# Optimization experiments

Hardware: AMD Instinct MI355X
Metric: run time of the kernel (lower is better)

## Reference

```python
import jax, jax.numpy as jnp
import numpy as np

N = 50000      # nodes
F_IN = 256     # nfeat
HID = 64       # nhid (per-head, layer 1)
H = 4          # heads layer 1
OUT = 64       # nhid2 (layer 2, heads=1, concat=False)
E = 800000     # edges (self-loops appended in reference)
NEG_SLOPE = 0.2  # PyG GATConv default LeakyReLU slope


def setup_inputs() -> dict:
    key = jax.random.key(0)
    ks = jax.random.split(key, 10)
    x = jax.random.normal(ks[0], (N, F_IN), dtype=jnp.float32)
    adj = jax.random.randint(ks[1], (2, E), 0, N)
    s1 = 1.0 / np.sqrt(F_IN)
    s2 = 1.0 / np.sqrt(H * HID)
    W1 = (jax.random.normal(ks[2], (F_IN, H * HID), dtype=jnp.float32) * s1)
    att_src1 = jax.random.normal(ks[3], (H, HID), dtype=jnp.float32) * 0.1
    att_dst1 = jax.random.normal(ks[4], (H, HID), dtype=jnp.float32) * 0.1
    b1 = jnp.zeros((H * HID,), dtype=jnp.float32)
    W2 = (jax.random.normal(ks[5], (H * HID, OUT), dtype=jnp.float32) * s2)
    att_src2 = jax.random.normal(ks[6], (1, OUT), dtype=jnp.float32) * 0.1
    att_dst2 = jax.random.normal(ks[7], (1, OUT), dtype=jnp.float32) * 0.1
    b2 = jnp.zeros((OUT,), dtype=jnp.float32)
    return {"x": x, "adj": adj, "W1": W1, "att_src1": att_src1,
            "att_dst1": att_dst1, "b1": b1, "W2": W2, "att_src2": att_src2,
            "att_dst2": att_dst2, "b2": b2}


def _gat_conv(x, src, dst, W, a_src, a_dst, bias, heads, out_ch, concat):
    n = x.shape[0]
    h = (x @ W).reshape(n, heads, out_ch)                    # [N, H, C]
    alpha_src = jnp.einsum('nhc,hc->nh', h, a_src)           # [N, H]
    alpha_dst = jnp.einsum('nhc,hc->nh', h, a_dst)           # [N, H]
    alpha = jax.nn.leaky_relu(alpha_src[src] + alpha_dst[dst],
                              negative_slope=NEG_SLOPE)      # [E, H]
    # segment softmax over incoming edges of each dst node
    m = jax.ops.segment_max(alpha, dst, num_segments=n)      # [N, H]
    e = jnp.exp(alpha - m[dst])
    denom = jax.ops.segment_sum(e, dst, num_segments=n)      # [N, H]
    a = e / denom[dst]                                       # [E, H]
    msg = h[src] * a[:, :, None]                             # [E, H, C]
    out = jax.ops.segment_sum(msg, dst, num_segments=n)      # [N, H, C]
    if concat:
        out = out.reshape(n, heads * out_ch)
    else:
        out = out.mean(axis=1)
    return out + bias


def reference(x, adj, W1, att_src1, att_dst1, b1, W2, att_src2, att_dst2, b2):
    loops = jnp.arange(N, dtype=adj.dtype)
    src = jnp.concatenate([adj[0], loops])
    dst = jnp.concatenate([adj[1], loops])
    h = _gat_conv(x, src, dst, W1, att_src1, att_dst1, b1, H, HID, True)
    h = jax.nn.elu(h)
    out = _gat_conv(h, src, dst, W2, att_src2, att_dst2, b2, 1, OUT, False)
    return jax.nn.log_softmax(out, axis=1)
```

## Files before the change

### kernel.cpp

```cpp
#include <hip/hip_runtime.h>
#include <cstdint>
#include <cstddef>

#define NN    50000
#define EE    800000
#define SLOPE 0.2f
#define MT64  782
#define CAP   64

#define NBIN  196
#define DSH   8
#define PBLK  1024
#define EPB   782
#define BCAP  14
#define OCAP  8192

typedef unsigned short ushortT;
typedef __attribute__((ext_vector_type(8))) short short8;
typedef __attribute__((ext_vector_type(4))) float floatx4;

__device__ __forceinline__ float lrelu(float x){ return x > 0.f ? x : SLOPE * x; }
__device__ __forceinline__ float eluf(float x){ return x > 0.f ? x : __expf(x) - 1.f; }
__device__ __forceinline__ ushortT f2b(float f){ unsigned u = __float_as_uint(f); u += 0x7fff + ((u >> 16) & 1); return (ushortT)(u >> 16); }
__device__ __forceinline__ float   b2f(ushortT b){ return __uint_as_float(((unsigned)b) << 16); }

__global__ __launch_bounds__(256) void castW_k(const float* __restrict__ W1, const float* __restrict__ W2,
                                               ushortT* __restrict__ W1T, ushortT* __restrict__ W2T,
                                               int* __restrict__ ovfcnt)
{
    int k = blockIdx.x, t = threadIdx.x;
    W1T[t * 256 + k] = f2b(W1[k * 256 + t]);
    if (t < 64) W2T[t * 256 + k] = f2b(W2[k * 64 + t]);
    if (k == 0 && t == 0) *ovfcnt = 0;
}

__global__ __launch_bounds__(256, 3) void gemmbin_k(const float* __restrict__ x,
                                                    const ushortT* __restrict__ W1T,
                                                    const float* __restrict__ attS,
                                                    const float* __restrict__ attD,
                                                    ushortT* __restrict__ h1b,
                                                    float* __restrict__ asrc,
                                                    float* __restrict__ adst,
                                                    const int* __restrict__ srcA,
                                                    const int* __restrict__ dstA,
                                                    unsigned* __restrict__ binned,
                                                    ushortT* __restrict__ cnt2,
                                                    unsigned* __restrict__ ovf,
                                                    int* __restrict__ ovfcnt)
{
    __shared__ int      hist[NBIN];
    __shared__ unsigned lrec[NBIN][BCAP];

    if (blockIdx.x >= MT64) {
        const int blk = blockIdx.x - MT64;
        const int tid = threadIdx.x;
        for (int i = tid; i < NBIN; i += 256) hist[i] = 0;
        __syncthreads();

        const int e0 = blk * EPB;
        const int e1 = min(e0 + EPB, EE);
        for (int e = e0 + tid; e < e1; e += 256) {
            int s = srcA[e], d = dstA[e];
            int bin = d >> DSH;
            unsigned rec = ((unsigned)s << DSH) | (unsigned)(d & 255);
            int r = atomicAdd(&hist[bin], 1);
            if (r < BCAP) lrec[bin][r] = rec;
            else {
                int o = atomicAdd(ovfcnt, 1);
                if (o < OCAP) ovf[o] = ((unsigned)s << 16) | (unsigned)d;
            }
        }
        __syncthreads();

        for (int b = tid; b < NBIN; b += 256)
            cnt2[(size_t)blk * NBIN + b] = (ushortT)min(hist[b], BCAP);
        for (int sIdx = tid; sIdx < NBIN * BCAP; sIdx += 256) {
            int b = sIdx / BCAP;
            int i = sIdx - b * BCAP;
            if (i < min(hist[b], BCAP))
                binned[((size_t)blk * NBIN + b) * BCAP + i] = lrec[b][i];
        }
        return;
    }

    const int tid  = threadIdx.x;
    const int w    = tid >> 6;
    const int lane = tid & 63;
    const int m16  = lane & 15;
    const int quad = lane >> 4;
    const int wr   = w >> 1;
    const int wc   = w & 1;
    const int rowbase = blockIdx.x * 64 + wr * 32;
    const int colbase = wc * 128;

    const long r0 = min(rowbase + m16,      NN - 1);
    const long r1 = min(rowbase + 16 + m16, NN - 1);
    const float* a0p = x + r0 * 256 + quad * 8;
    const float* a1p = x + r1 * 256 + quad * 8;
    const ushortT* bp0 = W1T + (size_t)(colbase + m16) * 256 + quad * 8;

    floatx4 acc[2][8];
    #pragma unroll
    for (int i = 0; i < 2; ++i)
        #pragma unroll
        for (int j = 0; j < 8; ++j) acc[i][j] = (floatx4){0.f, 0.f, 0.f, 0.f};

    #pragma unroll
    for (int it = 0; it < 8; ++it) {
        const int k0 = it * 32;
        float4 fa00 = *(const float4*)(a0p + k0);
        float4 fa01 = *(const float4*)(a0p + k0 + 4);
        float4 fa10 = *(const float4*)(a1p + k0);
        float4 fa11 = *(const float4*)(a1p + k0 + 4);
        uint4 fb[8];
        #pragma unroll
        for (int j = 0; j < 8; ++j)
            fb[j] = *(const uint4*)(bp0 + (size_t)j * 16 * 256 + k0);

        ushortT a16[16];
        a16[0]=f2b(fa00.x); a16[1]=f2b(fa00.y); a16[2]=f2b(fa00.z); a16[3]=f2b(fa00.w);
        a16[4]=f2b(fa01.x); a16[5]=f2b(fa01.y); a16[6]=f2b(fa01.z); a16[7]=f2b(fa01.w);
        a16[8]=f2b(fa10.x); a16[9]=f2b(fa10.y); a16[10]=f2b(fa10.z); a16[11]=f2b(fa10.w);
        a16[12]=f2b(fa11.x); a16[13]=f2b(fa11.y); a16[14]=f2b(fa11.z); a16[15]=f2b(fa11.w);
        short8 af0 = *(short8*)(a16);
        short8 af1 = *(short8*)(a16 + 8);

        #pragma unroll
        for (int j = 0; j < 8; ++j) {
            short8 bf = *(short8*)(&fb[j]);
            acc[0][j] = __builtin_amdgcn_mfma_f32_16x16x32_bf16(af0, bf, acc[0][j], 0, 0, 0);
            acc[1][j] = __builtin_amdgcn_mfma_f32_16x16x32_bf16(af1, bf, acc[1][j], 0, 0, 0);
        }
    }

    float attSv[8], attDv[8];
    #pragma unroll
    for (int j = 0; j < 8; ++j) {
        attSv[j] = attS[colbase + j * 16 + m16];
        attDv[j] = attD[colbase + j * 16 + m16];
    }

    #pragma unroll
    for (int i = 0; i < 2; ++i) {
        #pragma unroll
        for (int r = 0; r < 4; ++r) {
            int row = rowbase + i * 16 + quad * 4 + r;
            bool ok = row < NN;
            if (ok) {
                #pragma unroll
                for (int j = 0; j < 8; ++j)
                    h1b[(size_t)row * 256 + colbase + j * 16 + m16] = f2b(acc[i][j][r]);
            }
            float d0 = 0.f, d1 = 0.f, e0 = 0.f, e1 = 0.f;
            #pragma unroll
            for (int jj = 0; jj < 4; ++jj) {
                d0 += acc[i][jj][r]     * attSv[jj];
                e0 += acc[i][jj][r]     * attDv[jj];
                d1 += acc[i][jj + 4][r] * attSv[jj + 4];
                e1 += acc[i][jj + 4][r] * attDv[jj + 4];
            }
            #pragma unroll
            for (int off = 1; off < 16; off <<= 1) {
                d0 += __shfl_xor(d0, off); e0 += __shfl_xor(e0, off);
                d1 += __shfl_xor(d1, off); e1 += __shfl_xor(e1, off);
            }
            if (ok && m16 == 0) {
                int hb = row * 4 + wc * 2;
                asrc[hb] = d0; asrc[hb + 1] = d1;
                adst[hb] = e0; adst[hb + 1] = e1;
            }
        }
    }
}

__global__ __launch_bounds__(256) void bucket_k(const unsigned* __restrict__ binned,
                                                const ushortT* __restrict__ cnt2,
                                                const unsigned* __restrict__ ovf,
                                                const int* __restrict__ ovfcnt,
                                                ushortT* __restrict__ esorted,
                                                int* __restrict__ cnt)
{
    __shared__ ushortT c2[PBLK];
    __shared__ int     lcnt[256];
    __shared__ ushortT lbuck[256][CAP];
    const int b = blockIdx.x;
    const int tid = threadIdx.x;

    lcnt[tid] = 0;
    for (int i = tid; i < PBLK; i += 256) c2[i] = cnt2[(size_t)i * NBIN + b];
    __syncthreads();

    for (int s0 = tid; s0 < PBLK * BCAP; s0 += 1024) {
        unsigned recs[4]; int ok[4];
        #pragma unroll
        for (int q = 0; q < 4; ++q) {
            int s = s0 + q * 256;
            int blk = s / BCAP;
            int i = s - blk * BCAP;
            ok[q] = (i < (int)c2[blk]);
            recs[q] = ok[q] ? binned[((size_t)blk * NBIN + b) * BCAP + i] : 0u;
        }
        #pragma unroll
        for (int q = 0; q < 4; ++q) {
            if (ok[q]) {
                int dl = recs[q] & 255;
                int r = atomicAdd(&lcnt[dl], 1);
                if (r < CAP) lbuck[dl][r] = (ushortT)(recs[q] >> DSH);
            }
        }
    }

    int nov = *ovfcnt;
    nov = nov > OCAP ? OCAP : nov;
    for (int i = tid; i < nov; i += 256) {
        unsigned rec = ovf[i];
        int d = rec & 0xFFFF;
        if ((d >> DSH) == b) {
            int r = atomicAdd(&lcnt[d & 255], 1);
            if (r < CAP) lbuck[d & 255][r] = (ushortT)(rec >> 16);
        }
    }
    __syncthreads();

    const int nbase = b << DSH;
    {
        int n = nbase + tid;
        if (n < NN) cnt[n] = lcnt[tid];
    }
    unsigned* ed = (unsigned*)(esorted + (size_t)nbase * CAP);
    const unsigned* ls = (const unsigned*)(&lbuck[0][0]);
    for (int i = tid; i < 256 * (CAP / 2); i += 256) {
        if (nbase + (i >> 5) < NN) ed[i] = ls[i];
    }
}

__global__ __launch_bounds__(256) void gemm2_k(const ushortT* __restrict__ a2b,
                                               const ushortT* __restrict__ W2T,
                                               const float* __restrict__ attS,
                                               const float* __restrict__ attD,
                                               ushortT* __restrict__ t2b,
                                               float* __restrict__ asrc,
                                               float* __restrict__ adst)
{
    const int tid  = threadIdx.x;
    const int w    = tid >> 6;
    const int lane = tid & 63;
    const int m16  = lane & 15;
    const int quad = lane >> 4;
    const int rowbase = blockIdx.x * 64 + w * 16;

    const long r0 = min(rowbase + m16, NN - 1);
    const ushortT* ap  = a2b + r0 * 256 + quad * 8;
    const ushortT* bp0 = W2T + (size_t)m16 * 256 + quad * 8;

    floatx4 acc[4];
    #pragma unroll
    for (int j = 0; j < 4; ++j) acc[j] = (floatx4){0.f, 0.f, 0.f, 0.f};

    #pragma unroll
    for (int it = 0; it < 8; ++it) {
        const int k0 = it * 32;
        uint4 fa = *(const uint4*)(ap + k0);
        uint4 fb[4];
        #pragma unroll
        for (int j = 0; j < 4; ++j)
            fb[j] = *(const uint4*)(bp0 + (size_t)j * 16 * 256 + k0);
        short8 af = *(short8*)(&fa);
        #pragma unroll
        for (int j = 0; j < 4; ++j) {
            short8 bf = *(short8*)(&fb[j]);
            acc[j] = __builtin_amdgcn_mfma_f32_16x16x32_bf16(af, bf, acc[j], 0, 0, 0);
        }
    }

    float attSv[4], attDv[4];
    #pragma unroll
    for (int j = 0; j < 4; ++j) {
        attSv[j] = attS[j * 16 + m16];
        attDv[j] = attD[j * 16 + m16];
    }

    #pragma unroll
    for (int r = 0; r < 4; ++r) {
        int row = rowbase + quad * 4 + r;
        bool ok = row < NN;
        if (ok) {
            #pragma unroll
            for (int j = 0; j < 4; ++j)
                t2b[(size_t)row * 64 + j * 16 + m16] = f2b(acc[j][r]);
        }
        float ds = 0.f, dd = 0.f;
        #pragma unroll
        for (int j = 0; j < 4; ++j) {
            ds += acc[j][r] * attSv[j];
            dd += acc[j][r] * attDv[j];
        }
        #pragma unroll
        for (int off = 1; off < 16; off <<= 1) {
            ds += __shfl_xor(ds, off);
            dd += __shfl_xor(dd, off);
        }
        if (ok && m16 == 0) {
            asrc[row] = ds;
            adst[row] = dd;
        }
    }
}

__global__ __launch_bounds__(256) void agg1_k(const ushortT* __restrict__ esorted,
                                              const int* __restrict__ cnt,
                                              const ushortT* __restrict__ h1b,
                                              const float* __restrict__ asrc,
                                              const float* __restrict__ adst,
                                              const float* __restrict__ b1,
                                              ushortT* __restrict__ a2b)
{
    __shared__ float pbuf[4][64][4];
    __shared__ int   sbuf[4][64];
    int w = threadIdx.x >> 6;
    int lane = threadIdx.x & 63;
    int n = blockIdx.x * 4 + w;
    if (n >= NN) return;
    int start = n * CAP;
    int deg = min(max(cnt[n], 0), CAP);
    float4 adv = *(const float4*)(adst + (size_t)n * 4);
    float4 asf = *(const float4*)(asrc + (size_t)n * 4);
    int h = lane >> 4;
    int c4 = lane * 4;

    float4 pself;
    pself.x = __expf(lrelu(asf.x + adv.x));
    pself.y = __expf(lrelu(asf.y + adv.y));
    pself.z = __expf(lrelu(asf.z + adv.z));
    pself.w = __expf(lrelu(asf.w + adv.w));
    float psh = (h < 2) ? (h == 0 ? pself.x : pself.y) : (h == 2 ? pself.z : pself.w);

    ushort4 hsv = *(const ushort4*)(h1b + (size_t)n * 256 + c4);
    float4 ac0 = make_float4(b2f(hsv.x) * psh, b2f(hsv.y) * psh, b2f(hsv.z) * psh, b2f(hsv.w) * psh);
    float4 ac1 = make_float4(0.f,0.f,0.f,0.f);
    float4 ac2 = make_float4(0.f,0.f,0.f,0.f);
    float4 ac3 = make_float4(0.f,0.f,0.f,0.f);
    float4 ssv = make_float4(0.f, 0.f, 0.f, 0.f);

    if (lane < deg) {
        int s = esorted[start + lane];
        float4 a = *(const float4*)(asrc + (size_t)s * 4);
        float4 pv;
        pv.x = __expf(lrelu(a.x + adv.x));
        pv.y = __expf(lrelu(a.y + adv.y));
        pv.z = __expf(lrelu(a.z + adv.z));
        pv.w = __expf(lrelu(a.w + adv.w));
        ssv = pv;
        *(float4*)(&pbuf[w][lane][0]) = pv;
        sbuf[w][lane] = s;
    } else {
        *(float4*)(&pbuf[w][lane][0]) = make_float4(0.f, 0.f, 0.f, 0.f);
        sbuf[w][lane] = 0;
    }
    __builtin_amdgcn_wave_barrier();

    int nb = (deg + 7) >> 3;
    ushort4 bufA[8], bufB[8];

#define LOADR(BUF, J0) { _Pragma("unroll") for (int q = 0; q < 8; ++q) { \
        int sq = sbuf[w][(J0) + q]; \
        BUF[q] = *(const ushort4*)(h1b + (size_t)sq * 256 + c4); } }
#define CONSR(BUF, J0) { _Pragma("unroll") for (int q = 0; q < 8; ++q) { \
        float p = pbuf[w][(J0) + q][h]; \
        float4* ac = (q & 3) == 0 ? &ac0 : (q & 3) == 1 ? &ac1 : (q & 3) == 2 ? &ac2 : &ac3; \
        ac->x += b2f(BUF[q].x) * p; ac->y += b2f(BUF[q].y) * p; \
        ac->z += b2f(BUF[q].z) * p; ac->w += b2f(BUF[q].w) * p; } }

    if (nb > 0) {
        LOADR(bufA, 0)
        #pragma unroll
        for (int b = 0; b < 8; ++b) {
            const int j0 = b << 3;
            if (b & 1) {
                if (b + 1 < nb) LOADR(bufA, j0 + 8)
                CONSR(bufB, j0)
            } else {
                if (b + 1 < nb) LOADR(bufB, j0 + 8)
                CONSR(bufA, j0)
            }
            if (b + 1 >= nb) break;
        }
    }
#undef LOADR
#undef CONSR

    #pragma unroll
    for (int off = 1; off < 64; off <<= 1) {
        ssv.x += __shfl_xor(ssv.x, off); ssv.y += __shfl_xor(ssv.y, off);
        ssv.z += __shfl_xor(ssv.z, off); ssv.w += __shfl_xor(ssv.w, off);
    }
    float ssh = (h < 2) ? (h == 0 ? ssv.x : ssv.y) : (h == 2 ? ssv.z : ssv.w);
    float rdh = 1.f / (ssh + psh);

    float4 bv = *(const float4*)(b1 + c4);
    ushort4 o;
    o.x = f2b(eluf((ac0.x + ac1.x + ac2.x + ac3.x) * rdh + bv.x));
    o.y = f2b(eluf((ac0.y + ac1.y + ac2.y + ac3.y) * rdh + bv.y));
    o.z = f2b(eluf((ac0.z + ac1.z + ac2.z + ac3.z) * rdh + bv.z));
    o.w = f2b(eluf((ac0.w + ac1.w + ac2.w + ac3.w) * rdh + bv.w));
    *(ushort4*)(a2b + (size_t)n * 256 + c4) = o;
}

__global__ __launch_bounds__(256) void agg2_k(const ushortT* __restrict__ esorted,
                                              const int* __restrict__ cnt,
                                              const ushortT* __restrict__ t2b,
                                              const float* __restrict__ asrc,
                                              const float* __restrict__ adst,
                                              const float* __restrict__ b2,
                                              float* __restrict__ out)
{
    __shared__ float pbuf[4][64];
    __shared__ int   sbuf[4][64];
    int w = threadIdx.x >> 6;
    int lane = threadIdx.x & 63;
    int n = blockIdx.x * 4 + w;
    if (n >= NN) return;
    int start = n * CAP;
    int deg = min(max(cnt[n], 0), CAP);
    float adv = adst[n];

    float pself = __expf(lrelu(asrc[n] + adv));
    float a0 = b2f(t2b[(size_t)n * 64 + lane]) * pself;
    float a1 = 0.f, a2 = 0.f, a3 = 0.f;
    float ss = 0.f;

    if (lane < deg) {
        int s = esorted[start + lane];
        float p = __expf(lrelu(asrc[s] + adv));
        ss = p;
        pbuf[w][lane] = p;
        sbuf[w][lane] = s;
    } else {
        pbuf[w][lane] = 0.f;
        sbuf[w][lane] = 0;
    }
    __builtin_amdgcn_wave_barrier();

    int nb = (deg + 7) >> 3;
    ushortT bufA[8], bufB[8];

#define LOADR2(BUF, J0) { _Pragma("unroll") for (int q = 0; q < 8; ++q) { \
        int sq = sbuf[w][(J0) + q]; \
        BUF[q] = t2b[(size_t)sq * 64 + lane]; } }
#define CONSR2(BUF, J0) { _Pragma("unroll") for (int q = 0; q < 8; ++q) { \
        float p = pbuf[w][(J0) + q]; \
        float* ac = (q & 3) == 0 ? &a0 : (q & 3) == 1 ? &a1 : (q & 3) == 2 ? &a2 : &a3; \
        *ac += b2f(BUF[q]) * p; } }

    if (nb > 0) {
        LOADR2(bufA, 0)
        #pragma unroll
        for (int b = 0; b < 8; ++b) {
            const int j0 = b << 3;
            if (b & 1) {
                if (b + 1 < nb) LOADR2(bufA, j0 + 8)
                CONSR2(bufB, j0)
            } else {
                if (b + 1 < nb) LOADR2(bufB, j0 + 8)
                CONSR2(bufA, j0)
            }
            if (b + 1 >= nb) break;
        }
    }
#undef LOADR2
#undef CONSR2

    #pragma unroll
    for (int off = 1; off < 64; off <<= 1) ss += __shfl_xor(ss, off);
    float v = (a0 + a1 + a2 + a3) / (ss + pself) + b2[lane];

    float m2 = v;
    #pragma unroll
    for (int off = 32; off; off >>= 1) m2 = fmaxf(m2, __shfl_xor(m2, off));
    float ex = __expf(v - m2);
    float sm = ex;
    #pragma unroll
    for (int off = 32; off; off >>= 1) sm += __shfl_xor(sm, off);
    out[(size_t)n * 64 + lane] = v - m2 - __logf(sm);
}

extern "C" void kernel_launch(void* const* d_in, const int* in_sizes, int n_in,
                              void* d_out, int out_size, void* d_ws, size_t ws_size,
                              hipStream_t stream)
{
    const float* x   = (const float*)d_in[0];
    const int*   adj = (const int*)  d_in[1];
    const float* W1  = (const float*)d_in[2];
    const float* as1 = (const float*)d_in[3];
    const float* ad1 = (const float*)d_in[4];
    const float* b1  = (const float*)d_in[5];
    const float* W2  = (const float*)d_in[6];
    const float* as2 = (const float*)d_in[7];
    const float* ad2 = (const float*)d_in[8];
    const float* b2  = (const float*)d_in[9];
    float* out = (float*)d_out;

    const size_t szH1b = (size_t)NN * 256 * 2;
    const size_t szT2b = (size_t)NN * 64 * 2;
    const size_t szA4  = (size_t)NN * 4 * 4;
    const size_t szA1  = (size_t)NN * 4;
    const size_t szE   = (size_t)NN * CAP * 2;
    const size_t szBin = (size_t)NBIN * PBLK * BCAP * 4;
    const size_t szC2  = (size_t)PBLK * NBIN * 2;

    char* p = (char*)d_ws;
    ushortT* h1b  = (ushortT*)p; p += szH1b;
    ushortT* a2b  = (ushortT*)p; p += szH1b;
    ushortT* t2b  = (ushortT*)p; p += szT2b;
    ushortT* W1T  = (ushortT*)p; p += 256 * 256 * 2;
    ushortT* W2T  = (ushortT*)p; p += 64 * 256 * 2;
    float* asrc1  = (float*)p; p += szA4;
    float* adst1  = (float*)p; p += szA4;
    float* asrc2  = (float*)p; p += szA1;
    float* adst2  = (float*)p; p += szA1;
    ushortT* esorted = (ushortT*)p; p += szE;
    int* cnt      = (int*)p; p += szA1;
    unsigned* binned = (unsigned*)p; p += szBin;
    ushortT* cnt2 = (ushortT*)p; p += szC2;
    unsigned* ovf = (unsigned*)p; p += (size_t)OCAP * 4;
    int* ovfcnt   = (int*)p; p += 64;

    const int nwb = (NN + 3) / 4;

    castW_k<<<256, 256, 0, stream>>>(W1, W2, W1T, W2T, ovfcnt);

    gemmbin_k<<<MT64 + PBLK, 256, 0, stream>>>(x, W1T, as1, ad1, h1b, asrc1, adst1,
                                               adj, adj + EE, binned, cnt2, ovf, ovfcnt);

    bucket_k<<<NBIN, 256, 0, stream>>>(binned, cnt2, ovf, ovfcnt, esorted, cnt);

    agg1_k<<<nwb, 256, 0, stream>>>(esorted, cnt, h1b, asrc1, adst1, b1, a2b);
    gemm2_k<<<MT64, 256, 0, stream>>>(a2b, W2T, as2, ad2, t2b, asrc2, adst2);
    agg2_k<<<nwb, 256, 0, stream>>>(esorted, cnt, t2b, asrc2, adst2, b2, out);
}
```

Measured before the change: 280.6 us.

## Regroup kernels: fuse weight cast with edge binning, overlap bucketing with GEMM

New measurement: 267.1 us. 1.05x faster.

```diff
diff --git a/kernel.cpp b/kernel.cpp
--- a/kernel.cpp
+++ b/kernel.cpp
@@ -14,6 +14,8 @@
 #define EPB   782
 #define BCAP  14
 #define OCAP  8192
+#define CASTB 20
+#define BUCKB NBIN
 
 typedef unsigned short ushortT;
 typedef __attribute__((ext_vector_type(8))) short short8;
@@ -24,73 +26,162 @@
 __device__ __forceinline__ ushortT f2b(float f){ unsigned u = __float_as_uint(f); u += 0x7fff + ((u >> 16) & 1); return (ushortT)(u >> 16); }
 __device__ __forceinline__ float   b2f(ushortT b){ return __uint_as_float(((unsigned)b) << 16); }
 
-__global__ __launch_bounds__(256) void castW_k(const float* __restrict__ W1, const float* __restrict__ W2,
-                                               ushortT* __restrict__ W1T, ushortT* __restrict__ W2T,
-                                               int* __restrict__ ovfcnt)
-{
-    int k = blockIdx.x, t = threadIdx.x;
-    W1T[t * 256 + k] = f2b(W1[k * 256 + t]);
-    if (t < 64) W2T[t * 256 + k] = f2b(W2[k * 64 + t]);
-    if (k == 0 && t == 0) *ovfcnt = 0;
-}
-
-__global__ __launch_bounds__(256, 3) void gemmbin_k(const float* __restrict__ x,
-                                                    const ushortT* __restrict__ W1T,
-                                                    const float* __restrict__ attS,
-                                                    const float* __restrict__ attD,
-                                                    ushortT* __restrict__ h1b,
-                                                    float* __restrict__ asrc,
-                                                    float* __restrict__ adst,
-                                                    const int* __restrict__ srcA,
+__global__ __launch_bounds__(256, 3) void binCast_k(const int* __restrict__ srcA,
                                                     const int* __restrict__ dstA,
                                                     unsigned* __restrict__ binned,
                                                     ushortT* __restrict__ cnt2,
                                                     unsigned* __restrict__ ovf,
-                                                    int* __restrict__ ovfcnt)
+                                                    int* __restrict__ ovfcnt,
+                                                    const float* __restrict__ W1,
+                                                    const float* __restrict__ W2,
+                                                    ushortT* __restrict__ W1T,
+                                                    ushortT* __restrict__ W2T)
 {
+    __shared__ float    tile[64][65];
     __shared__ int      hist[NBIN];
     __shared__ unsigned lrec[NBIN][BCAP];
 
-    if (blockIdx.x >= MT64) {
-        const int blk = blockIdx.x - MT64;
-        const int tid = threadIdx.x;
-        for (int i = tid; i < NBIN; i += 256) hist[i] = 0;
+    const int tid = threadIdx.x;
+    if (blockIdx.x < CASTB) {
+        const int lr = tid >> 6;
+        const int lc = tid & 63;
+        if (blockIdx.x < 16) {
+            const int tr = blockIdx.x >> 2, tc = blockIdx.x & 3;
+            #pragma unroll
+            for (int i = 0; i < 16; ++i) {
+                int r = lr + i * 4;
+                tile[r][lc] = W1[(size_t)(tr * 64 + r) * 256 + tc * 64 + lc];
+            }
+            __syncthreads();
+            #pragma unroll
+            for (int i = 0; i < 16; ++i) {
+                int r = lr + i * 4;
+                W1T[(size_t)(tc * 64 + r) * 256 + tr * 64 + lc] = f2b(tile[lc][r]);
+            }
+        } else {
+            const int tk = blockIdx.x - 16;
+            #pragma unroll
+            for (int i = 0; i < 16; ++i) {
+                int r = lr + i * 4;
+                tile[r][lc] = W2[(size_t)(tk * 64 + r) * 64 + lc];
+            }
+            __syncthreads();
+            #pragma unroll
+            for (int i = 0; i < 16; ++i) {
+                int r = lr + i * 4;
+                W2T[(size_t)r * 256 + tk * 64 + lc] = f2b(tile[lc][r]);
+            }
+        }
+        return;
+    }
+
+    const int blk = blockIdx.x - CASTB;
+    for (int i = tid; i < NBIN; i += 256) hist[i] = 0;
+    __syncthreads();
+
+    const int e0 = blk * EPB;
+    const int e1 = min(e0 + EPB, EE);
+    for (int e = e0 + tid; e < e1; e += 256) {
+        int s = srcA[e], d = dstA[e];
+        int bin = d >> DSH;
+        unsigned rec = ((unsigned)s << DSH) | (unsigned)(d & 255);
+        int r = atomicAdd(&hist[bin], 1);
+        if (r < BCAP) lrec[bin][r] = rec;
+        else {
+            int o = atomicAdd(ovfcnt, 1);
+            if (o < OCAP) ovf[o] = ((unsigned)s << 16) | (unsigned)d;
+        }
+    }
+    __syncthreads();
+
+    for (int b = tid; b < NBIN; b += 256)
+        cnt2[(size_t)blk * NBIN + b] = (ushortT)min(hist[b], BCAP);
+    for (int sIdx = tid; sIdx < NBIN * BCAP; sIdx += 256) {
+        int b = sIdx / BCAP;
+        int i = sIdx - b * BCAP;
+        if (i < min(hist[b], BCAP))
+            binned[((size_t)blk * NBIN + b) * BCAP + i] = lrec[b][i];
+    }
+}
+
+__global__ __launch_bounds__(256, 3) void gembucket_k(const float* __restrict__ x,
+                                                      const ushortT* __restrict__ W1T,
+                                                      const float* __restrict__ attS,
+                                                      const float* __restrict__ attD,
+                                                      ushortT* __restrict__ h1b,
+                                                      float* __restrict__ asrc,
+                                                      float* __restrict__ adst,
+                                                      const unsigned* __restrict__ binned,
+                                                      const ushortT* __restrict__ cnt2,
+                                                      const unsigned* __restrict__ ovf,
+                                                      const int* __restrict__ ovfcnt,
+                                                      ushortT* __restrict__ esorted,
+                                                      int* __restrict__ cnt)
+{
+    __shared__ ushortT c2[PBLK];
+    __shared__ int     lcnt[256];
+    __shared__ ushortT lbuck[256][CAP];
+
+    const int tid = threadIdx.x;
+    if (blockIdx.x < BUCKB) {
+        const int b = blockIdx.x;
+        lcnt[tid] = 0;
+        for (int i = tid; i < PBLK; i += 256) c2[i] = cnt2[(size_t)i * NBIN + b];
         __syncthreads();
 
-        const int e0 = blk * EPB;
-        const int e1 = min(e0 + EPB, EE);
-        for (int e = e0 + tid; e < e1; e += 256) {
-            int s = srcA[e], d = dstA[e];
-            int bin = d >> DSH;
-            unsigned rec = ((unsigned)s << DSH) | (unsigned)(d & 255);
-            int r = atomicAdd(&hist[bin], 1);
-            if (r < BCAP) lrec[bin][r] = rec;
-            else {
-                int o = atomicAdd(ovfcnt, 1);
-                if (o < OCAP) ovf[o] = ((unsigned)s << 16) | (unsigned)d;
+        for (int s0 = tid; s0 < PBLK * BCAP; s0 += 2048) {
+            unsigned recs[8]; int ok[8];
+            #pragma unroll
+            for (int q = 0; q < 8; ++q) {
+                int s = s0 + q * 256;
+                int blk = s / BCAP;
+                int i = s - blk * BCAP;
+                ok[q] = (i < (int)c2[blk]);
+                recs[q] = ok[q] ? binned[((size_t)blk * NBIN + b) * BCAP + i] : 0u;
+            }
+            #pragma unroll
+            for (int q = 0; q < 8; ++q) {
+                if (ok[q]) {
+                    int dl = recs[q] & 255;
+                    int r = atomicAdd(&lcnt[dl], 1);
+                    if (r < CAP) lbuck[dl][r] = (ushortT)(recs[q] >> DSH);
+                }
+            }
+        }
+
+        int nov = *ovfcnt;
+        nov = nov > OCAP ? OCAP : nov;
+        for (int i = tid; i < nov; i += 256) {
+            unsigned rec = ovf[i];
+            int d = rec & 0xFFFF;
+            if ((d >> DSH) == b) {
+                int r = atomicAdd(&lcnt[d & 255], 1);
+                if (r < CAP) lbuck[d & 255][r] = (ushortT)(rec >> 16);
             }
         }
         __syncthreads();
 
-        for (int b = tid; b < NBIN; b += 256)
-            cnt2[(size_t)blk * NBIN + b] = (ushortT)min(hist[b], BCAP);
-        for (int sIdx = tid; sIdx < NBIN * BCAP; sIdx += 256) {
-            int b = sIdx / BCAP;
-            int i = sIdx - b * BCAP;
-            if (i < min(hist[b], BCAP))
-                binned[((size_t)blk * NBIN + b) * BCAP + i] = lrec[b][i];
+        const int nbase = b << DSH;
+        {
+            int n = nbase + tid;
+            if (n < NN) cnt[n] = lcnt[tid];
+        }
+        unsigned* ed = (unsigned*)(esorted + (size_t)nbase * CAP);
+        const unsigned* ls = (const unsigned*)(&lbuck[0][0]);
+        for (int i = tid; i < 256 * (CAP / 2); i += 256) {
+            if (nbase + (i >> 5) < NN) ed[i] = ls[i];
         }
         return;
     }
 
-    const int tid  = threadIdx.x;
     const int w    = tid >> 6;
     const int lane = tid & 63;
     const int m16  = lane & 15;
     const int quad = lane >> 4;
     const int wr   = w >> 1;
     const int wc   = w & 1;
-    const int rowbase = blockIdx.x * 64 + wr * 32;
+    const int gb   = blockIdx.x - BUCKB;
+    const int rowbase = gb * 64 + wr * 32;
     const int colbase = wc * 128;
 
     const long r0 = min(rowbase + m16,      NN - 1);
@@ -170,67 +261,6 @@
                 adst[hb] = e0; adst[hb + 1] = e1;
             }
         }
-    }
-}
-
-__global__ __launch_bounds__(256) void bucket_k(const unsigned* __restrict__ binned,
-                                                const ushortT* __restrict__ cnt2,
-                                                const unsigned* __restrict__ ovf,
-                                                const int* __restrict__ ovfcnt,
-                                                ushortT* __restrict__ esorted,
-                                                int* __restrict__ cnt)
-{
-    __shared__ ushortT c2[PBLK];
-    __shared__ int     lcnt[256];
-    __shared__ ushortT lbuck[256][CAP];
-    const int b = blockIdx.x;
-    const int tid = threadIdx.x;
-
-    lcnt[tid] = 0;
-    for (int i = tid; i < PBLK; i += 256) c2[i] = cnt2[(size_t)i * NBIN + b];
-    __syncthreads();
-
-    for (int s0 = tid; s0 < PBLK * BCAP; s0 += 1024) {
-        unsigned recs[4]; int ok[4];
-        #pragma unroll
-        for (int q = 0; q < 4; ++q) {
-            int s = s0 + q * 256;
-            int blk = s / BCAP;
-            int i = s - blk * BCAP;
-            ok[q] = (i < (int)c2[blk]);
-            recs[q] = ok[q] ? binned[((size_t)blk * NBIN + b) * BCAP + i] : 0u;
-        }
-        #pragma unroll
-        for (int q = 0; q < 4; ++q) {
-            if (ok[q]) {
-                int dl = recs[q] & 255;
-                int r = atomicAdd(&lcnt[dl], 1);
-                if (r < CAP) lbuck[dl][r] = (ushortT)(recs[q] >> DSH);
-            }
-        }
-    }
-
-    int nov = *ovfcnt;
-    nov = nov > OCAP ? OCAP : nov;
-    for (int i = tid; i < nov; i += 256) {
-        unsigned rec = ovf[i];
-        int d = rec & 0xFFFF;
-        if ((d >> DSH) == b) {
-            int r = atomicAdd(&lcnt[d & 255], 1);
-            if (r < CAP) lbuck[d & 255][r] = (ushortT)(rec >> 16);
-        }
-    }
-    __syncthreads();
-
-    const int nbase = b << DSH;
-    {
-        int n = nbase + tid;
-        if (n < NN) cnt[n] = lcnt[tid];
-    }
-    unsigned* ed = (unsigned*)(esorted + (size_t)nbase * CAP);
-    const unsigned* ls = (const unsigned*)(&lbuck[0][0]);
-    for (int i = tid; i < 256 * (CAP / 2); i += 256) {
-        if (nbase + (i >> 5) < NN) ed[i] = ls[i];
     }
 }
 
@@ -527,12 +557,13 @@
 
     const int nwb = (NN + 3) / 4;
 
-    castW_k<<<256, 256, 0, stream>>>(W1, W2, W1T, W2T, ovfcnt);
-
-    gemmbin_k<<<MT64 + PBLK, 256, 0, stream>>>(x, W1T, as1, ad1, h1b, asrc1, adst1,
-                                               adj, adj + EE, binned, cnt2, ovf, ovfcnt);
-
-    bucket_k<<<NBIN, 256, 0, stream>>>(binned, cnt2, ovf, ovfcnt, esorted, cnt);
+    hipMemsetAsync(ovfcnt, 0, sizeof(int), stream);
+
+    binCast_k<<<CASTB + PBLK, 256, 0, stream>>>(adj, adj + EE, binned, cnt2, ovf, ovfcnt,
+                                                W1, W2, W1T, W2T);
+
+    gembucket_k<<<BUCKB + MT64, 256, 0, stream>>>(x, W1T, as1, ad1, h1b, asrc1, adst1,
+                                                  binned, cnt2, ovf, ovfcnt, esorted, cnt);
 
     agg1_k<<<nwb, 256, 0, stream>>>(esorted, cnt, h1b, asrc1, adst1, b1, a2b);
     gemm2_k<<<MT64, 256, 0, stream>>>(a2b, W2T, as2, ad2, t2b, asrc2, adst2);
```
